# Kernel tuning notes

Hardware: AMD Instinct MI355X
Metric: run time of the kernel (lower is better)

## Reference

```python
import jax, jax.numpy as jnp
import numpy as np


def setup_inputs() -> dict:
    key = jax.random.key(0)
    x = jax.random.normal(key, (1024, 65536), dtype=jnp.float32)
    return {"x": x, "k": 64}


def reference(x, k):
    # BatchTopK: ReLU, then keep the k*batch largest activations across the
    # ENTIRE flattened batch, zeroing everything else.
    acts = jax.nn.relu(x)
    flat = acts.reshape(-1)                      # [batch * d_sae]
    k_total = k * x.shape[0]
    vals, idx = jax.lax.top_k(flat, k_total)     # global selection
    out = jnp.zeros_like(flat).at[idx].set(vals) # scatter back
    return out.reshape(acts.shape)
```

## Files before the change

### kernel.cpp

```cpp
#include <hip/hip_runtime.h>
#include <stdint.h>


#define HDR_CURSOR 0
#define HDR_FLAG   1
#define HDR_THR    2
#define HDR_ICUT   3
#define HIST_OFF   4096
#define CAND_OFF   16384
#define NBINS      2048u
#define BUCKET_CAP 6144u
#define SCAN_STAGE 1024
#define ROWS       1024u
#define SPEC       3.0f
#define BASE_BITS  0x40400000u

typedef float f32x4 __attribute__((ext_vector_type(4)));

__device__ __forceinline__ uint32_t bin_of(uint32_t key) {
  uint32_t off = key - BASE_BITS;
  uint32_t b = off >> 12;
  return b < NBINS ? b : (NBINS - 1u);
}

__device__ __forceinline__ float max4(float4 a) {
  return fmaxf(fmaxf(a.x, a.y), fmaxf(a.z, a.w));
}

__global__ void k_init(uint32_t* hdr, uint32_t* ghist, uint32_t force_flag) {
  for (uint32_t i = threadIdx.x; i < 64u + NBINS; i += 256u) {
    if (i < 64u) hdr[i] = 0u;
    else ghist[i - 64u] = 0u;
  }
  if (threadIdx.x == 0u) hdr[HDR_FLAG] = force_flag;
}

__device__ __forceinline__ void push4(float4 a, uint32_t gi,
                                      uint32_t* s_cnt, uint2* s_buf) {
  if (a.x >= SPEC) { uint32_t p = atomicAdd(s_cnt, 1u); if (p < SCAN_STAGE) s_buf[p] = make_uint2(__float_as_uint(a.x), gi); }
  if (a.y >= SPEC) { uint32_t p = atomicAdd(s_cnt, 1u); if (p < SCAN_STAGE) s_buf[p] = make_uint2(__float_as_uint(a.y), gi + 1u); }
  if (a.z >= SPEC) { uint32_t p = atomicAdd(s_cnt, 1u); if (p < SCAN_STAGE) s_buf[p] = make_uint2(__float_as_uint(a.z), gi + 2u); }
  if (a.w >= SPEC) { uint32_t p = atomicAdd(s_cnt, 1u); if (p < SCAN_STAGE) s_buf[p] = make_uint2(__float_as_uint(a.w), gi + 3u); }
}

__global__ __launch_bounds__(256) void k_scan(
    const float4* __restrict__ x4, const float* __restrict__ x,
    uint2* __restrict__ cand, uint32_t* __restrict__ hdr,
    uint32_t* __restrict__ ghist,
    uint32_t cap, uint32_t n4, uint32_t n) {
  __shared__ uint32_t s_cnt;
  __shared__ uint32_t s_base;
  __shared__ uint2 s_buf[SCAN_STAGE];
  if (threadIdx.x == 0u) s_cnt = 0u;
  __syncthreads();

  uint32_t stride = gridDim.x * blockDim.x;
  uint32_t i = blockIdx.x * blockDim.x + threadIdx.x;
  for (; i + 7u * stride < n4; i += 8u * stride) {
    float4 a0 = x4[i];
    float4 a1 = x4[i + stride];
    float4 a2 = x4[i + 2u * stride];
    float4 a3 = x4[i + 3u * stride];
    float4 a4 = x4[i + 4u * stride];
    float4 a5 = x4[i + 5u * stride];
    float4 a6 = x4[i + 6u * stride];
    float4 a7 = x4[i + 7u * stride];
    float m0 = max4(a0), m1 = max4(a1), m2 = max4(a2), m3 = max4(a3);
    float m4 = max4(a4), m5 = max4(a5), m6 = max4(a6), m7 = max4(a7);
    if (__ballot(m0 >= SPEC)) push4(a0, (i) * 4u, &s_cnt, s_buf);
    if (__ballot(m1 >= SPEC)) push4(a1, (i + stride) * 4u, &s_cnt, s_buf);
    if (__ballot(m2 >= SPEC)) push4(a2, (i + 2u * stride) * 4u, &s_cnt, s_buf);
    if (__ballot(m3 >= SPEC)) push4(a3, (i + 3u * stride) * 4u, &s_cnt, s_buf);
    if (__ballot(m4 >= SPEC)) push4(a4, (i + 4u * stride) * 4u, &s_cnt, s_buf);
    if (__ballot(m5 >= SPEC)) push4(a5, (i + 5u * stride) * 4u, &s_cnt, s_buf);
    if (__ballot(m6 >= SPEC)) push4(a6, (i + 6u * stride) * 4u, &s_cnt, s_buf);
    if (__ballot(m7 >= SPEC)) push4(a7, (i + 7u * stride) * 4u, &s_cnt, s_buf);
  }
  for (; i < n4; i += stride) {
    float4 a = x4[i];
    if (__ballot(max4(a) >= SPEC)) push4(a, i * 4u, &s_cnt, s_buf);
  }
  uint32_t tail0 = n4 * 4u;
  if (blockIdx.x == 0u && threadIdx.x < (n - tail0)) {
    uint32_t gi = tail0 + threadIdx.x;
    float v = x[gi];
    if (v >= SPEC) { uint32_t p = atomicAdd(&s_cnt, 1u); if (p < SCAN_STAGE) s_buf[p] = make_uint2(__float_as_uint(v), gi); }
  }
  __syncthreads();
  uint32_t cnt = s_cnt;
  if (cnt == 0u) return;
  uint32_t wcnt = cnt < (uint32_t)SCAN_STAGE ? cnt : (uint32_t)SCAN_STAGE;
  if (threadIdx.x == 0u) {
    s_base = atomicAdd(&hdr[HDR_CURSOR], cnt);
    if (cnt > (uint32_t)SCAN_STAGE) atomicOr(&hdr[HDR_FLAG], 1u);
  }
  __syncthreads();
  uint32_t base = s_base;
  for (uint32_t j = threadIdx.x; j < wcnt; j += blockDim.x) {
    uint32_t gidx = base + j;
    if (gidx < cap) {
      uint2 c = s_buf[j];
      cand[gidx] = c;
      atomicAdd(&ghist[bin_of(c.x)], 1u);
    }
  }
  if (threadIdx.x == 0u && base + wcnt > cap) atomicOr(&hdr[HDR_FLAG], 1u);
}

__global__ __launch_bounds__(256) void k_zero(
    float4* __restrict__ out4, float* __restrict__ out,
    uint32_t n4, uint32_t n) {
  const f32x4 z = {0.f, 0.f, 0.f, 0.f};
  uint32_t stride = gridDim.x * blockDim.x;
  uint32_t i = blockIdx.x * blockDim.x + threadIdx.x;
#pragma unroll 4
  for (; i < n4; i += stride)
    __builtin_nontemporal_store(z, (f32x4*)(out4 + i));
  uint32_t tail0 = n4 * 4u;
  if (blockIdx.x == 0u && threadIdx.x < (n - tail0))
    out[tail0 + threadIdx.x] = 0.f;
}

__global__ __launch_bounds__(1024) void k_select(
    const uint2* __restrict__ cand, uint32_t* __restrict__ hdr,
    const uint32_t* __restrict__ ghist,
    const int* __restrict__ kptr, uint32_t cap) {
  __shared__ uint32_t h[NBINS];
  __shared__ uint32_t s_sel, s_rank, s_bcnt;
  __shared__ uint2 bkt[BUCKET_CAP];
  uint32_t tid = threadIdx.x;
  uint32_t K = (uint32_t)kptr[0] * ROWS;
  uint32_t M = hdr[HDR_CURSOR];
  if (hdr[HDR_FLAG] != 0u || M > cap || M < K) {
    if (tid == 0u) hdr[HDR_FLAG] = 1u;
    return;
  }
  if (K == 0u) {
    if (tid == 0u) { hdr[HDR_THR] = 0xFFFFFFFFu; hdr[HDR_ICUT] = 0xFFFFFFFFu; }
    return;
  }
  h[tid] = ghist[tid];
  h[tid + 1024u] = ghist[tid + 1024u];
  if (tid == 0u) s_bcnt = 0u;
  __syncthreads();
  if (tid < 64u) {
    uint32_t seg = NBINS >> 6;
    uint32_t base = tid * seg;
    uint32_t lanesum = 0u;
    for (uint32_t j = 0; j < seg; ++j) lanesum += h[base + j];
    uint32_t s = lanesum;
    for (int d = 1; d < 64; d <<= 1) {
      uint32_t v = (uint32_t)__shfl_down((int)s, d, 64);
      if ((int)tid + d < 64) s += v;
    }
    uint32_t above = s - lanesum;
    if (above < K && above + lanesum >= K) {
      uint32_t r = K - above;
      uint32_t cum = 0u;
      for (int j = (int)seg - 1; j >= 0; --j) {
        uint32_t c = h[base + (uint32_t)j];
        if (cum + c >= r) { s_sel = base + (uint32_t)j; s_rank = r - cum; break; }
        cum += c;
      }
    }
  }
  __syncthreads();
  uint32_t bsel = s_sel;
  uint32_t r = s_rank;
  uint32_t E = h[bsel];
  if (bsel == NBINS - 1u || E > BUCKET_CAP) {
    if (tid == 0u) hdr[HDR_FLAG] = 1u;
    return;
  }
  const uint4* __restrict__ cand4 = (const uint4*)cand;
  uint32_t M2 = M >> 1;
  uint32_t j = tid;
  for (; j + 3072u < M2; j += 4096u) {
    uint4 c0 = cand4[j];
    uint4 c1 = cand4[j + 1024u];
    uint4 c2 = cand4[j + 2048u];
    uint4 c3 = cand4[j + 3072u];
    if (bin_of(c0.x) == bsel) { uint32_t p = atomicAdd(&s_bcnt, 1u); if (p < BUCKET_CAP) bkt[p] = make_uint2(c0.x, c0.y); }
    if (bin_of(c0.z) == bsel) { uint32_t p = atomicAdd(&s_bcnt, 1u); if (p < BUCKET_CAP) bkt[p] = make_uint2(c0.z, c0.w); }
    if (bin_of(c1.x) == bsel) { uint32_t p = atomicAdd(&s_bcnt, 1u); if (p < BUCKET_CAP) bkt[p] = make_uint2(c1.x, c1.y); }
    if (bin_of(c1.z) == bsel) { uint32_t p = atomicAdd(&s_bcnt, 1u); if (p < BUCKET_CAP) bkt[p] = make_uint2(c1.z, c1.w); }
    if (bin_of(c2.x) == bsel) { uint32_t p = atomicAdd(&s_bcnt, 1u); if (p < BUCKET_CAP) bkt[p] = make_uint2(c2.x, c2.y); }
    if (bin_of(c2.z) == bsel) { uint32_t p = atomicAdd(&s_bcnt, 1u); if (p < BUCKET_CAP) bkt[p] = make_uint2(c2.z, c2.w); }
    if (bin_of(c3.x) == bsel) { uint32_t p = atomicAdd(&s_bcnt, 1u); if (p < BUCKET_CAP) bkt[p] = make_uint2(c3.x, c3.y); }
    if (bin_of(c3.z) == bsel) { uint32_t p = atomicAdd(&s_bcnt, 1u); if (p < BUCKET_CAP) bkt[p] = make_uint2(c3.z, c3.w); }
  }
  for (; j < M2; j += 1024u) {
    uint4 c = cand4[j];
    if (bin_of(c.x) == bsel) { uint32_t p = atomicAdd(&s_bcnt, 1u); if (p < BUCKET_CAP) bkt[p] = make_uint2(c.x, c.y); }
    if (bin_of(c.z) == bsel) { uint32_t p = atomicAdd(&s_bcnt, 1u); if (p < BUCKET_CAP) bkt[p] = make_uint2(c.z, c.w); }
  }
  if (tid == 0u && (M & 1u)) {
    uint2 c = cand[M - 1u];
    if (bin_of(c.x) == bsel) { uint32_t p = atomicAdd(&s_bcnt, 1u); if (p < BUCKET_CAP) bkt[p] = c; }
  }
  __syncthreads();
  for (uint32_t e = tid; e < E; e += 1024u) {
    uint2 me = bkt[e];
    uint32_t rank = 0u;
    for (uint32_t jj = 0; jj < E; ++jj) {
      uint2 o = bkt[jj];
      rank += (o.x > me.x || (o.x == me.x && o.y < me.y)) ? 1u : 0u;
    }
    if (rank == r - 1u) { hdr[HDR_THR] = me.x; hdr[HDR_ICUT] = me.y; }
  }
}

__global__ __launch_bounds__(256) void k_scatter(
    const uint2* __restrict__ cand, const uint32_t* __restrict__ hdr,
    float* __restrict__ out, uint32_t cap) {
  if (hdr[HDR_FLAG] != 0u) return;
  uint32_t M = hdr[HDR_CURSOR]; if (M > cap) M = cap;
  uint32_t thr = hdr[HDR_THR], icut = hdr[HDR_ICUT];
  uint32_t stride = gridDim.x * blockDim.x;
  for (uint32_t i = blockIdx.x * blockDim.x + threadIdx.x; i < M; i += stride) {
    uint2 c = cand[i];
    if (c.x > thr || (c.x == thr && c.y <= icut)) out[c.y] = __uint_as_float(c.x);
  }
}

__global__ __launch_bounds__(1024) void k_fallback(
    const float* __restrict__ x, float* __restrict__ out,
    const int* __restrict__ kptr, const uint32_t* __restrict__ hdr, uint32_t n) {
  if (hdr[HDR_FLAG] == 0u) return;
  __shared__ uint32_t hist[2048];
  __shared__ uint32_t s_sel, s_rank, s_found, s_eqcnt, s_icut;
  __shared__ uint32_t eq_idx[4096];
  uint32_t tid = threadIdx.x;
  uint32_t K = (uint32_t)kptr[0] * ROWS;
  uint32_t prefix = 0u;
  uint32_t R = K;
  bool zero_thr = (K == 0u);
  for (int lvl = 0; lvl < 3 && !zero_thr; ++lvl) {
    uint32_t shift = (lvl == 0) ? 21u : (lvl == 1 ? 10u : 0u);
    uint32_t nb = (lvl == 2) ? 1024u : 2048u;
    for (uint32_t b = tid; b < nb; b += 1024u) hist[b] = 0u;
    __syncthreads();
    for (uint32_t i = tid; i < n; i += 1024u) {
      float v = x[i];
      uint32_t key = (v > 0.f) ? __float_as_uint(v) : 0u;
      bool valid = (key != 0u);
      if (lvl == 1) valid = valid && ((key >> 21) == prefix);
      if (lvl == 2) valid = valid && ((key >> 10) == prefix);
      if (valid) atomicAdd(&hist[(key >> shift) & (nb - 1u)], 1u);
    }
    __syncthreads();
    if (tid == 0u) {
      uint32_t cum = 0u, sel = 0u, rr = R, found = 0u;
      for (int b = (int)nb - 1; b >= 0; --b) {
        uint32_t c = hist[b];
        if (cum + c >= R) { sel = (uint32_t)b; rr = R - cum; found = 1u; break; }
        cum += c;
      }
      s_sel = sel; s_rank = rr; s_found = found;
    }
    __syncthreads();
    if (s_found == 0u) {
      zero_thr = true;
    } else {
      uint32_t sel = s_sel;
      R = s_rank;
      if (lvl == 0) prefix = sel;
      else if (lvl == 1) prefix = (prefix << 11) | sel;
      else prefix = (prefix << 10) | sel;
    }
    __syncthreads();
  }
  uint32_t thr_key = zero_thr ? 0u : prefix;
  uint32_t icut = 0xFFFFFFFFu;
  if (!zero_thr) {
    uint32_t E = hist[thr_key & 1023u];
    uint32_t T = R;
    if (T < E) {
      if (tid == 0u) { s_eqcnt = 0u; s_icut = 0xFFFFFFFFu; }
      __syncthreads();
      for (uint32_t i = tid; i < n; i += 1024u) {
        float v = x[i];
        if (v > 0.f && __float_as_uint(v) == thr_key) {
          uint32_t p = atomicAdd(&s_eqcnt, 1u);
          if (p < 4096u) eq_idx[p] = i;
        }
      }
      __syncthreads();
      uint32_t ec = s_eqcnt < 4096u ? s_eqcnt : 4096u;
      for (uint32_t e = tid; e < ec; e += 1024u) {
        uint32_t me = eq_idx[e];
        uint32_t rank = 0u;
        for (uint32_t j = 0; j < ec; ++j) rank += (eq_idx[j] < me) ? 1u : 0u;
        if (rank == T - 1u) s_icut = me;
      }
      __syncthreads();
      icut = s_icut;
    }
  }
  for (uint32_t i = tid; i < n; i += 1024u) {
    float v = x[i];
    uint32_t key = (v > 0.f) ? __float_as_uint(v) : 0u;
    bool keep = (key > thr_key) || (key != 0u && key == thr_key && i <= icut);
    out[i] = keep ? v : 0.f;
  }
}

extern "C" void kernel_launch(void* const* d_in, const int* in_sizes, int n_in,
                              void* d_out, int out_size, void* d_ws, size_t ws_size,
                              hipStream_t stream) {
  const float* x = (const float*)d_in[0];
  const int* kptr = (const int*)d_in[1];
  float* out = (float*)d_out;
  uint32_t n = (uint32_t)in_sizes[0];
  uint32_t n4 = n >> 2;

  uint32_t* hdr = (uint32_t*)d_ws;
  uint32_t* ghist = (uint32_t*)((char*)d_ws + HIST_OFF);
  uint2* cand = (uint2*)((char*)d_ws + CAND_OFF);
  uint32_t cap = (ws_size > (size_t)CAND_OFF) ? (uint32_t)((ws_size - CAND_OFF) / 8) : 0u;
  uint32_t force = (cap < 131072u) ? 1u : 0u;

  k_init<<<1, 256, 0, stream>>>(hdr, ghist, force);
  k_scan<<<2048, 256, 0, stream>>>((const float4*)x, x, cand, hdr, ghist, cap, n4, n);
  k_zero<<<2048, 256, 0, stream>>>((float4*)out, out, n4, n);
  k_select<<<1, 1024, 0, stream>>>(cand, hdr, ghist, kptr, cap);
  k_fallback<<<1, 1024, 0, stream>>>(x, out, kptr, hdr, n);
  k_scatter<<<512, 256, 0, stream>>>(cand, hdr, out, cap);
}
```

Baseline: 508.6 us.

## Fuse scan, zeroing, selection and scatter into one kernel with last-block finish

The output zeroing is merged into the input scan loop, so a single grid pass reads x and writes zeros. The last block to finish, detected with an atomic done-counter and thread fences, then runs the histogram bucket selection and the candidate scatter itself. This removes three kernel launches, the inter-kernel gaps and a separate pass over the output. In exchange, selection and scatter now run on one 256-thread block, serialising a scatter that used to be spread over 512 blocks. The bucket capacity is also shrunk to 1024 to fit shared memory, which sends more cases to the slow fallback path.

```diff
diff --git a/kernel.cpp b/kernel.cpp
--- a/kernel.cpp
+++ b/kernel.cpp
@@ -6,10 +6,11 @@
 #define HDR_FLAG   1
 #define HDR_THR    2
 #define HDR_ICUT   3
+#define HDR_DONE   4
 #define HIST_OFF   4096
 #define CAND_OFF   16384
 #define NBINS      2048u
-#define BUCKET_CAP 6144u
+#define BUCKET_CAP 1024u
 #define SCAN_STAGE 1024
 #define ROWS       1024u
 #define SPEC       3.0f
@@ -25,6 +26,10 @@
 
 __device__ __forceinline__ float max4(float4 a) {
   return fmaxf(fmaxf(a.x, a.y), fmaxf(a.z, a.w));
+}
+
+__device__ __forceinline__ uint32_t aload(uint32_t* p) {
+  return atomicAdd(p, 0u);
 }
 
 __global__ void k_init(uint32_t* hdr, uint32_t* ghist, uint32_t force_flag) {
@@ -43,19 +48,24 @@
   if (a.w >= SPEC) { uint32_t p = atomicAdd(s_cnt, 1u); if (p < SCAN_STAGE) s_buf[p] = make_uint2(__float_as_uint(a.w), gi + 3u); }
 }
 
-__global__ __launch_bounds__(256) void k_scan(
+__global__ __launch_bounds__(256) void k_fused(
+    float4* __restrict__ out4, float* __restrict__ out,
     const float4* __restrict__ x4, const float* __restrict__ x,
     uint2* __restrict__ cand, uint32_t* __restrict__ hdr,
-    uint32_t* __restrict__ ghist,
+    uint32_t* __restrict__ ghist, const int* __restrict__ kptr,
     uint32_t cap, uint32_t n4, uint32_t n) {
-  __shared__ uint32_t s_cnt;
-  __shared__ uint32_t s_base;
-  __shared__ uint2 s_buf[SCAN_STAGE];
-  if (threadIdx.x == 0u) s_cnt = 0u;
-  __syncthreads();
-
+  __shared__ uint32_t s_cnt, s_base, s_last, s_sel, s_rank, s_bcnt, s_thr, s_icut;
+  __shared__ __align__(16) uint8_t s_mem[16384];
+  uint2* s_buf = (uint2*)s_mem;
+  uint32_t* h = (uint32_t*)s_mem;
+  uint2* bkt = (uint2*)(s_mem + 8192);
+  uint32_t tid = threadIdx.x;
+  if (tid == 0u) s_cnt = 0u;
+  __syncthreads();
+
+  const f32x4 z = {0.f, 0.f, 0.f, 0.f};
   uint32_t stride = gridDim.x * blockDim.x;
-  uint32_t i = blockIdx.x * blockDim.x + threadIdx.x;
+  uint32_t i = blockIdx.x * blockDim.x + tid;
   for (; i + 7u * stride < n4; i += 8u * stride) {
     float4 a0 = x4[i];
     float4 a1 = x4[i + stride];
@@ -65,6 +75,14 @@
     float4 a5 = x4[i + 5u * stride];
     float4 a6 = x4[i + 6u * stride];
     float4 a7 = x4[i + 7u * stride];
+    __builtin_nontemporal_store(z, (f32x4*)(out4 + i));
+    __builtin_nontemporal_store(z, (f32x4*)(out4 + i + stride));
+    __builtin_nontemporal_store(z, (f32x4*)(out4 + i + 2u * stride));
+    __builtin_nontemporal_store(z, (f32x4*)(out4 + i + 3u * stride));
+    __builtin_nontemporal_store(z, (f32x4*)(out4 + i + 4u * stride));
+    __builtin_nontemporal_store(z, (f32x4*)(out4 + i + 5u * stride));
+    __builtin_nontemporal_store(z, (f32x4*)(out4 + i + 6u * stride));
+    __builtin_nontemporal_store(z, (f32x4*)(out4 + i + 7u * stride));
     float m0 = max4(a0), m1 = max4(a1), m2 = max4(a2), m3 = max4(a3);
     float m4 = max4(a4), m5 = max4(a5), m6 = max4(a6), m7 = max4(a7);
     if (__ballot(m0 >= SPEC)) push4(a0, (i) * 4u, &s_cnt, s_buf);
@@ -78,69 +96,58 @@
   }
   for (; i < n4; i += stride) {
     float4 a = x4[i];
+    __builtin_nontemporal_store(z, (f32x4*)(out4 + i));
     if (__ballot(max4(a) >= SPEC)) push4(a, i * 4u, &s_cnt, s_buf);
   }
   uint32_t tail0 = n4 * 4u;
-  if (blockIdx.x == 0u && threadIdx.x < (n - tail0)) {
-    uint32_t gi = tail0 + threadIdx.x;
+  if (blockIdx.x == 0u && tid < (n - tail0)) {
+    uint32_t gi = tail0 + tid;
     float v = x[gi];
+    out[gi] = 0.f;
     if (v >= SPEC) { uint32_t p = atomicAdd(&s_cnt, 1u); if (p < SCAN_STAGE) s_buf[p] = make_uint2(__float_as_uint(v), gi); }
   }
   __syncthreads();
+
   uint32_t cnt = s_cnt;
-  if (cnt == 0u) return;
-  uint32_t wcnt = cnt < (uint32_t)SCAN_STAGE ? cnt : (uint32_t)SCAN_STAGE;
-  if (threadIdx.x == 0u) {
-    s_base = atomicAdd(&hdr[HDR_CURSOR], cnt);
-    if (cnt > (uint32_t)SCAN_STAGE) atomicOr(&hdr[HDR_FLAG], 1u);
-  }
-  __syncthreads();
-  uint32_t base = s_base;
-  for (uint32_t j = threadIdx.x; j < wcnt; j += blockDim.x) {
-    uint32_t gidx = base + j;
-    if (gidx < cap) {
-      uint2 c = s_buf[j];
-      cand[gidx] = c;
-      atomicAdd(&ghist[bin_of(c.x)], 1u);
-    }
-  }
-  if (threadIdx.x == 0u && base + wcnt > cap) atomicOr(&hdr[HDR_FLAG], 1u);
-}
-
-__global__ __launch_bounds__(256) void k_zero(
-    float4* __restrict__ out4, float* __restrict__ out,
-    uint32_t n4, uint32_t n) {
-  const f32x4 z = {0.f, 0.f, 0.f, 0.f};
-  uint32_t stride = gridDim.x * blockDim.x;
-  uint32_t i = blockIdx.x * blockDim.x + threadIdx.x;
-#pragma unroll 4
-  for (; i < n4; i += stride)
-    __builtin_nontemporal_store(z, (f32x4*)(out4 + i));
-  uint32_t tail0 = n4 * 4u;
-  if (blockIdx.x == 0u && threadIdx.x < (n - tail0))
-    out[tail0 + threadIdx.x] = 0.f;
-}
-
-__global__ __launch_bounds__(1024) void k_select(
-    const uint2* __restrict__ cand, uint32_t* __restrict__ hdr,
-    const uint32_t* __restrict__ ghist,
-    const int* __restrict__ kptr, uint32_t cap) {
-  __shared__ uint32_t h[NBINS];
-  __shared__ uint32_t s_sel, s_rank, s_bcnt;
-  __shared__ uint2 bkt[BUCKET_CAP];
-  uint32_t tid = threadIdx.x;
+  if (cnt != 0u) {
+    uint32_t wcnt = cnt < (uint32_t)SCAN_STAGE ? cnt : (uint32_t)SCAN_STAGE;
+    if (tid == 0u) {
+      s_base = atomicAdd(&hdr[HDR_CURSOR], cnt);
+      if (cnt > (uint32_t)SCAN_STAGE) atomicOr(&hdr[HDR_FLAG], 1u);
+    }
+    __syncthreads();
+    uint32_t base = s_base;
+    for (uint32_t j = tid; j < wcnt; j += blockDim.x) {
+      uint32_t gidx = base + j;
+      if (gidx < cap) {
+        uint2 c = s_buf[j];
+        cand[gidx] = c;
+        atomicAdd(&ghist[bin_of(c.x)], 1u);
+      }
+    }
+    if (tid == 0u && base + wcnt > cap) atomicOr(&hdr[HDR_FLAG], 1u);
+  }
+
+  __threadfence();
+  __syncthreads();
+  if (tid == 0u) {
+    uint32_t d = atomicAdd(&hdr[HDR_DONE], 1u);
+    s_last = (d == gridDim.x - 1u) ? 1u : 0u;
+  }
+  __syncthreads();
+  if (s_last == 0u) return;
+  __threadfence();
+
   uint32_t K = (uint32_t)kptr[0] * ROWS;
-  uint32_t M = hdr[HDR_CURSOR];
-  if (hdr[HDR_FLAG] != 0u || M > cap || M < K) {
-    if (tid == 0u) hdr[HDR_FLAG] = 1u;
+  uint32_t M = aload(&hdr[HDR_CURSOR]);
+  uint32_t flag = aload(&hdr[HDR_FLAG]);
+  if (flag != 0u || M > cap || M < K) {
+    if (tid == 0u) atomicOr(&hdr[HDR_FLAG], 1u);
     return;
   }
-  if (K == 0u) {
-    if (tid == 0u) { hdr[HDR_THR] = 0xFFFFFFFFu; hdr[HDR_ICUT] = 0xFFFFFFFFu; }
-    return;
-  }
-  h[tid] = ghist[tid];
-  h[tid + 1024u] = ghist[tid + 1024u];
+  if (K == 0u) return;
+
+  for (uint32_t b = tid; b < NBINS; b += 256u) h[b] = ghist[b];
   if (tid == 0u) s_bcnt = 0u;
   __syncthreads();
   if (tid < 64u) {
@@ -169,17 +176,17 @@
   uint32_t r = s_rank;
   uint32_t E = h[bsel];
   if (bsel == NBINS - 1u || E > BUCKET_CAP) {
-    if (tid == 0u) hdr[HDR_FLAG] = 1u;
+    if (tid == 0u) atomicOr(&hdr[HDR_FLAG], 1u);
     return;
   }
   const uint4* __restrict__ cand4 = (const uint4*)cand;
   uint32_t M2 = M >> 1;
   uint32_t j = tid;
-  for (; j + 3072u < M2; j += 4096u) {
+  for (; j + 768u < M2; j += 1024u) {
     uint4 c0 = cand4[j];
-    uint4 c1 = cand4[j + 1024u];
-    uint4 c2 = cand4[j + 2048u];
-    uint4 c3 = cand4[j + 3072u];
+    uint4 c1 = cand4[j + 256u];
+    uint4 c2 = cand4[j + 512u];
+    uint4 c3 = cand4[j + 768u];
     if (bin_of(c0.x) == bsel) { uint32_t p = atomicAdd(&s_bcnt, 1u); if (p < BUCKET_CAP) bkt[p] = make_uint2(c0.x, c0.y); }
     if (bin_of(c0.z) == bsel) { uint32_t p = atomicAdd(&s_bcnt, 1u); if (p < BUCKET_CAP) bkt[p] = make_uint2(c0.z, c0.w); }
     if (bin_of(c1.x) == bsel) { uint32_t p = atomicAdd(&s_bcnt, 1u); if (p < BUCKET_CAP) bkt[p] = make_uint2(c1.x, c1.y); }
@@ -189,7 +196,7 @@
     if (bin_of(c3.x) == bsel) { uint32_t p = atomicAdd(&s_bcnt, 1u); if (p < BUCKET_CAP) bkt[p] = make_uint2(c3.x, c3.y); }
     if (bin_of(c3.z) == bsel) { uint32_t p = atomicAdd(&s_bcnt, 1u); if (p < BUCKET_CAP) bkt[p] = make_uint2(c3.z, c3.w); }
   }
-  for (; j < M2; j += 1024u) {
+  for (; j < M2; j += 256u) {
     uint4 c = cand4[j];
     if (bin_of(c.x) == bsel) { uint32_t p = atomicAdd(&s_bcnt, 1u); if (p < BUCKET_CAP) bkt[p] = make_uint2(c.x, c.y); }
     if (bin_of(c.z) == bsel) { uint32_t p = atomicAdd(&s_bcnt, 1u); if (p < BUCKET_CAP) bkt[p] = make_uint2(c.z, c.w); }
@@ -199,27 +206,25 @@
     if (bin_of(c.x) == bsel) { uint32_t p = atomicAdd(&s_bcnt, 1u); if (p < BUCKET_CAP) bkt[p] = c; }
   }
   __syncthreads();
-  for (uint32_t e = tid; e < E; e += 1024u) {
+  for (uint32_t e = tid; e < E; e += 256u) {
     uint2 me = bkt[e];
     uint32_t rank = 0u;
     for (uint32_t jj = 0; jj < E; ++jj) {
       uint2 o = bkt[jj];
       rank += (o.x > me.x || (o.x == me.x && o.y < me.y)) ? 1u : 0u;
     }
-    if (rank == r - 1u) { hdr[HDR_THR] = me.x; hdr[HDR_ICUT] = me.y; }
-  }
-}
-
-__global__ __launch_bounds__(256) void k_scatter(
-    const uint2* __restrict__ cand, const uint32_t* __restrict__ hdr,
-    float* __restrict__ out, uint32_t cap) {
-  if (hdr[HDR_FLAG] != 0u) return;
-  uint32_t M = hdr[HDR_CURSOR]; if (M > cap) M = cap;
-  uint32_t thr = hdr[HDR_THR], icut = hdr[HDR_ICUT];
-  uint32_t stride = gridDim.x * blockDim.x;
-  for (uint32_t i = blockIdx.x * blockDim.x + threadIdx.x; i < M; i += stride) {
-    uint2 c = cand[i];
-    if (c.x > thr || (c.x == thr && c.y <= icut)) out[c.y] = __uint_as_float(c.x);
+    if (rank == r - 1u) { s_thr = me.x; s_icut = me.y; hdr[HDR_THR] = me.x; hdr[HDR_ICUT] = me.y; }
+  }
+  __syncthreads();
+
+  uint32_t thr = s_thr, icut = s_icut;
+  float* sink = (float*)&hdr[48];
+#pragma unroll 8
+  for (uint32_t q = tid; q < M; q += 256u) {
+    uint2 c = cand[q];
+    bool keep = (c.x > thr) || (c.x == thr && c.y <= icut);
+    float* p = keep ? &out[c.y] : sink;
+    *p = __uint_as_float(c.x);
   }
 }
 
@@ -321,9 +326,7 @@
   uint32_t force = (cap < 131072u) ? 1u : 0u;
 
   k_init<<<1, 256, 0, stream>>>(hdr, ghist, force);
-  k_scan<<<2048, 256, 0, stream>>>((const float4*)x, x, cand, hdr, ghist, cap, n4, n);
-  k_zero<<<2048, 256, 0, stream>>>((float4*)out, out, n4, n);
-  k_select<<<1, 1024, 0, stream>>>(cand, hdr, ghist, kptr, cap);
+  k_fused<<<2048, 256, 0, stream>>>((float4*)out, out, (const float4*)x, x,
+                                    cand, hdr, ghist, kptr, cap, n4, n);
   k_fallback<<<1, 1024, 0, stream>>>(x, out, kptr, hdr, n);
-  k_scatter<<<512, 256, 0, stream>>>(cand, hdr, out, cap);
-}
+}
```

Result: slower. 973.3 us (+91.4%).
